# Performance work log

Hardware: AMD Instinct MI355X
Metric: run time of the kernel (lower is better)

The kernel has to match this reference:

```python
import jax, jax.numpy as jnp
import numpy as np

PT, SKIP, CNN_UNITS, RNN_UNITS = 16, 32, 512, 512


def setup_inputs() -> dict:
    key = jax.random.key(0)
    k_x, k_w, k_u = jax.random.split(key, 3)
    B, T, C, H = 128, 512, CNN_UNITS, RNN_UNITS
    # 0.05 scaling keeps the relu GRU recurrence numerically stable
    x = jax.random.normal(k_x, (B, T, C), dtype=jnp.float32)
    W = jax.random.normal(k_w, (C, 3 * H), dtype=jnp.float32) * 0.05
    U = jax.random.normal(k_u, (H, 3 * H), dtype=jnp.float32) * 0.05
    b = jnp.zeros((2, 3 * H), dtype=jnp.float32)  # [input_bias, recurrent_bias] (reset_after=True)
    return {"x": x, "W": W, "U": U, "b": b}


def reference(x, W, U, b):
    B, T, C = x.shape
    H = U.shape[0]
    pt, skip = PT, SKIP
    # pretrans: last pt*skip steps -> (B, pt, skip, C) -> (B, skip, pt, C) -> (B*skip, pt, C)
    s = x[:, -pt * skip:, :]
    s = s.reshape(B, pt, skip, C).transpose(0, 2, 1, 3).reshape(B * skip, pt, C)
    # precompute input projections for all timesteps: (pt, B*skip, 3H)
    xp = jnp.einsum('ntc,ch->tnh', s, W) + b[0]
    b_rec = b[1]

    def step(h, xt):
        rec = h @ U + b_rec                      # (N, 3H)
        xz, xr, xh = jnp.split(xt, 3, axis=-1)
        rz, rr, rh = jnp.split(rec, 3, axis=-1)
        z = jax.nn.sigmoid(xz + rz)
        r = jax.nn.sigmoid(xr + rr)
        hh = jax.nn.relu(xh + r * rh)            # activation='relu'
        h_new = z * h + (1.0 - z) * hh
        return h_new, None

    h0 = jnp.zeros((B * skip, H), dtype=x.dtype)
    h_final, _ = jax.lax.scan(step, h0, xp)
    # posttrans: (B*skip, H) -> (B, skip*H)
    return h_final.reshape(B, skip * H)
```

## Files before the change

### kernel.cpp

```cpp
#include <hip/hip_runtime.h>
#include <cstddef>


typedef unsigned short u16;
typedef __attribute__((ext_vector_type(8))) short short8;
typedef __attribute__((ext_vector_type(8))) u16 u16x8;
typedef __attribute__((ext_vector_type(4))) float floatx4;

#define MFMA16(a, b, c) __builtin_amdgcn_mfma_f32_16x16x32_bf16((a), (b), (c), 0, 0, 0)

__device__ __forceinline__ u16 f32_to_bf16(float f) {
  union { float f; unsigned int u; } c; c.f = f;
  unsigned int u = c.u + 0x7FFFu + ((c.u >> 16) & 1u);
  return (u16)(u >> 16);
}
__device__ __forceinline__ float bf16_to_f32(u16 v) {
  union { unsigned int u; float f; } c; c.u = ((unsigned int)v) << 16;
  return c.f;
}
__device__ __forceinline__ float sigmoidf_(float x) {
  return 1.0f / (1.0f + __expf(-x));
}
__device__ __forceinline__ void gload_lds16(const void* g, void* l) {
  __builtin_amdgcn_global_load_lds(
      (const __attribute__((address_space(1))) unsigned int*)g,
      (__attribute__((address_space(3))) unsigned int*)l, 16, 0, 0);
}

__global__ __launch_bounds__(256)
void pack_x(const float* __restrict__ x, u16* __restrict__ xb) {
  __shared__ u16 sm[64 * 512];
  const int t = blockIdx.x >> 6;
  const int nb = blockIdx.x & 63;
  const int tid = threadIdx.x;
#pragma unroll
  for (int it = 0; it < 16; ++it) {
    int idx = it * 256 + tid;
    int row = idx >> 6, ch = idx & 63;
    int xrow = (nb * 2 + (row >> 5)) * 512 + t * 32 + (row & 31);
    const float* src = x + (size_t)xrow * 512 + ch * 8;
    floatx4 va = *(const floatx4*)src;
    floatx4 vb = *(const floatx4*)(src + 4);
    u16x8 pk;
    pk[0] = f32_to_bf16(va[0]); pk[1] = f32_to_bf16(va[1]);
    pk[2] = f32_to_bf16(va[2]); pk[3] = f32_to_bf16(va[3]);
    pk[4] = f32_to_bf16(vb[0]); pk[5] = f32_to_bf16(vb[1]);
    pk[6] = f32_to_bf16(vb[2]); pk[7] = f32_to_bf16(vb[3]);
    *(u16x8*)&sm[row * 512 + (ch ^ (row & 7)) * 8] = pk;
  }
  __syncthreads();
  u16* dst = xb + (size_t)blockIdx.x * 32768;
#pragma unroll
  for (int it = 0; it < 16; ++it) {
    int idx = it * 256 + tid;
    int row = idx & 63, g = (idx >> 6) & 3, kt = idx >> 8;
    int ch = kt * 4 + g;
    u16x8 vv = *(const u16x8*)&sm[row * 512 + (ch ^ (row & 7)) * 8];
    *(u16x8*)(dst + (size_t)idx * 8) = vv;
  }
}

__global__ void pack_Bt(const float* __restrict__ W, const float* __restrict__ U,
                        u16* __restrict__ Bt) {
  size_t gid = (size_t)blockIdx.x * 256 + threadIdx.x;
  int col = (int)(gid & 63);
  int g   = (int)((gid >> 6) & 3);
  int kt  = (int)((gid >> 8) & 31);
  int cc  = (int)(gid >> 13);
  int c = cc * 64 + col;
  int k0 = kt * 32 + g * 8;
  u16x8 pk;
#pragma unroll
  for (int j = 0; j < 8; ++j) {
    int k = k0 + j;
    float v = (k < 512) ? W[(size_t)k * 1536 + c] : U[(size_t)(k - 512) * 1536 + c];
    pk[j] = f32_to_bf16(v);
  }
  *(u16x8*)(Bt + gid * 8) = pk;
}

__global__ __launch_bounds__(256)
void gru_step(const u16* __restrict__ xb, const u16* __restrict__ Bt,
              const float* __restrict__ bias,
              const u16* __restrict__ h_in, u16* __restrict__ h_out,
              float* __restrict__ out, int t, int first, int last) {
  __shared__ alignas(16) char sm[65536];
  const int tid = threadIdx.x;
  const int idx = blockIdx.x;
  const int nb = ((idx >> 6) << 3) | (idx & 7);
  const int hb = (idx >> 3) & 7;
  const int w = __builtin_amdgcn_readfirstlane(tid >> 6);
  const int lane = tid & 63;
  const int wy = w >> 1, wx = w & 1;
  const int q = lane >> 4, lc = lane & 15;

  const u16* xbB = xb + (size_t)(t * 64 + nb) * 32768;
  const u16* htB = h_in + (size_t)nb * 32768;
  const int cs0 = hb, cs1 = 8 + hb, cs2 = 16 + hb;

  floatx4 acZ[2][2] = {{{0.f,0.f,0.f,0.f},{0.f,0.f,0.f,0.f}},{{0.f,0.f,0.f,0.f},{0.f,0.f,0.f,0.f}}};
  floatx4 acR[2][2] = {{{0.f,0.f,0.f,0.f},{0.f,0.f,0.f,0.f}},{{0.f,0.f,0.f,0.f},{0.f,0.f,0.f,0.f}}};
  floatx4 acX[2][2] = {{{0.f,0.f,0.f,0.f},{0.f,0.f,0.f,0.f}},{{0.f,0.f,0.f,0.f},{0.f,0.f,0.f,0.f}}};
  floatx4 acH[2][2] = {{{0.f,0.f,0.f,0.f},{0.f,0.f,0.f,0.f}},{{0.f,0.f,0.f,0.f},{0.f,0.f,0.f,0.f}}};

  const int wo = w * 1024;

  auto stage = [&](int kt, int bsel) {
    char* lds = sm + bsel * 16384;
    const char* aS = (const char*)((kt < 16) ? (xbB + (size_t)kt * 2048)
                                             : (htB + (size_t)(kt - 16) * 2048));
    gload_lds16(aS + wo + lane * 16, lds + wo);
    gload_lds16((const char*)(Bt + (size_t)(cs0 * 32 + kt) * 2048) + wo + lane * 16,
                lds + 4096 + wo);
    gload_lds16((const char*)(Bt + (size_t)(cs1 * 32 + kt) * 2048) + wo + lane * 16,
                lds + 8192 + wo);
    gload_lds16((const char*)(Bt + (size_t)(cs2 * 32 + kt) * 2048) + wo + lane * 16,
                lds + 12288 + wo);
  };

  auto compute = [&](int bsel, floatx4 (&acT)[2][2]) {
    const char* lds = sm + bsel * 16384;
    short8 a0 = *(const short8*)(lds + (q * 64 + wy * 32 + lc) * 16);
    short8 a1 = *(const short8*)(lds + (q * 64 + wy * 32 + 16 + lc) * 16);
#pragma unroll
    for (int ci = 0; ci < 2; ++ci) {
      int co = (q * 64 + wx * 32 + ci * 16 + lc) * 16;
      short8 bz = *(const short8*)(lds + 4096 + co);
      short8 br = *(const short8*)(lds + 8192 + co);
      short8 bh = *(const short8*)(lds + 12288 + co);
      acZ[0][ci] = MFMA16(a0, bz, acZ[0][ci]);
      acZ[1][ci] = MFMA16(a1, bz, acZ[1][ci]);
      acR[0][ci] = MFMA16(a0, br, acR[0][ci]);
      acR[1][ci] = MFMA16(a1, br, acR[1][ci]);
      acT[0][ci] = MFMA16(a0, bh, acT[0][ci]);
      acT[1][ci] = MFMA16(a1, bh, acT[1][ci]);
    }
  };

  stage(0, 0);
  stage(1, 1);
  stage(2, 2);
  if (first) {
    for (int kt = 0; kt < 14; ++kt) {
      asm volatile("s_waitcnt vmcnt(8)" ::: "memory");
      __builtin_amdgcn_s_barrier();
      if (kt < 13) stage(kt + 3, (kt + 3) & 3);
      __builtin_amdgcn_s_setprio(1);
      compute(kt & 3, acX);
      __builtin_amdgcn_s_setprio(0);
    }
    asm volatile("s_waitcnt vmcnt(4)" ::: "memory");
    __builtin_amdgcn_s_barrier();
    __builtin_amdgcn_s_setprio(1);
    compute(2, acX);
    __builtin_amdgcn_s_setprio(0);
    asm volatile("s_waitcnt vmcnt(0)" ::: "memory");
    __builtin_amdgcn_s_barrier();
    __builtin_amdgcn_s_setprio(1);
    compute(3, acX);
    __builtin_amdgcn_s_setprio(0);
  } else {
    for (int kt = 0; kt < 16; ++kt) {
      asm volatile("s_waitcnt vmcnt(8)" ::: "memory");
      __builtin_amdgcn_s_barrier();
      stage(kt + 3, (kt + 3) & 3);
      __builtin_amdgcn_s_setprio(1);
      compute(kt & 3, acX);
      __builtin_amdgcn_s_setprio(0);
    }
    for (int kt = 16; kt < 30; ++kt) {
      asm volatile("s_waitcnt vmcnt(8)" ::: "memory");
      __builtin_amdgcn_s_barrier();
      if (kt < 29) stage(kt + 3, (kt + 3) & 3);
      __builtin_amdgcn_s_setprio(1);
      compute(kt & 3, acH);
      __builtin_amdgcn_s_setprio(0);
    }
    asm volatile("s_waitcnt vmcnt(4)" ::: "memory");
    __builtin_amdgcn_s_barrier();
    __builtin_amdgcn_s_setprio(1);
    compute(2, acH);
    __builtin_amdgcn_s_setprio(0);
    asm volatile("s_waitcnt vmcnt(0)" ::: "memory");
    __builtin_amdgcn_s_barrier();
    __builtin_amdgcn_s_setprio(1);
    compute(3, acH);
    __builtin_amdgcn_s_setprio(0);
  }

  __syncthreads();
  const float* b0 = bias;
  const float* b1 = bias + 1536;
  u16* Ct = (u16*)sm;
#pragma unroll
  for (int ci = 0; ci < 2; ++ci) {
    const int hcl = wx * 32 + ci * 16 + lc;
    const int hg = hb * 64 + hcl;
    const float bz = b0[hg] + b1[hg];
    const float br = b0[512 + hg] + b1[512 + hg];
    const float b0h = b0[1024 + hg];
    const float b1h = b1[1024 + hg];
    const int ktg = hg >> 5;
    const int gg = (hg >> 3) & 3;
    const size_t hbase = (((size_t)nb * 16 + ktg) * 4 + gg) * 64;
#pragma unroll
    for (int mi = 0; mi < 2; ++mi) {
#pragma unroll
      for (int reg = 0; reg < 4; ++reg) {
        const int nl = wy * 32 + mi * 16 + q * 4 + reg;
        const int n = nb * 64 + nl;
        float z = sigmoidf_(acZ[mi][ci][reg] + bz);
        float r = sigmoidf_(acR[mi][ci][reg] + br);
        float hh = acX[mi][ci][reg] + b0h + r * (acH[mi][ci][reg] + b1h);
        hh = fmaxf(hh, 0.0f);
        float hp = 0.0f;
        if (!first) hp = bf16_to_f32(h_in[(hbase + nl) * 8 + (hg & 7)]);
        float v = z * hp + (1.0f - z) * hh;
        if (last) out[(size_t)n * 512 + hg] = v;
        else      Ct[nl * 72 + hcl] = f32_to_bf16(v);
      }
    }
  }
  if (!last) {
    __syncthreads();
#pragma unroll
    for (int i = 0; i < 2; ++i) {
      int e = i * 256 + tid;
      int row = e & 63;
      int g = (e >> 6) & 3;
      int ktl = e >> 8;
      u16x8 vv = *(const u16x8*)(Ct + row * 72 + ktl * 32 + g * 8);
      *(u16x8*)(h_out + ((((size_t)nb * 16 + (hb * 2 + ktl)) * 4 + g) * 64 + row) * 8) = vv;
    }
  }
}

extern "C" void kernel_launch(void* const* d_in, const int* in_sizes, int n_in,
                              void* d_out, int out_size, void* d_ws, size_t ws_size,
                              hipStream_t stream) {
  const float* x = (const float*)d_in[0];
  const float* W = (const float*)d_in[1];
  const float* U = (const float*)d_in[2];
  const float* bias = (const float*)d_in[3];
  float* out = (float*)d_out;

  u16* xb = (u16*)d_ws;
  u16* Bt = xb + (size_t)16 * 64 * 32768;
  u16* h0 = Bt + (size_t)1536 * 1024;
  u16* h1 = h0 + (size_t)4096 * 512;

  pack_x<<<1024, 256, 0, stream>>>(x, xb);
  pack_Bt<<<768, 256, 0, stream>>>(W, U, Bt);

  for (int t = 0; t < 16; ++t) {
    const u16* hin = (t & 1) ? h1 : h0;
    u16* hout = (t & 1) ? h0 : h1;
    gru_step<<<512, 256, 0, stream>>>(
        xb, Bt, bias, hin, hout, out, t, (t == 0) ? 1 : 0, (t == 15) ? 1 : 0);
  }
}
```

Baseline: 503.6 us.

## Hoist input projection into one batched GEMM before recurrent steps

Moves the x·W input projection for all 16 timesteps out of the sequential per-step kernels into a single large 8192-block GEMM that writes fp32 results to workspace. Each gru_step then only does the h·U recurrent GEMM (K=512 instead of 1024) and reads the precomputed projections in its epilogue. This gives the input GEMM full-GPU parallelism instead of 512 blocks per step, and halves the serial critical path. The cost is an extra fp32 intermediate buffer (about 400MB written and read back) and the assumption that the workspace is large enough to hold it.

```diff
diff --git a/kernel.cpp b/kernel.cpp
--- a/kernel.cpp
+++ b/kernel.cpp
@@ -80,8 +80,94 @@
 }
 
 __global__ __launch_bounds__(256)
-void gru_step(const u16* __restrict__ xb, const u16* __restrict__ Bt,
-              const float* __restrict__ bias,
+void xw_gemm(const u16* __restrict__ xb, const u16* __restrict__ Bt,
+             float* __restrict__ xp) {
+  __shared__ alignas(16) char sm[65536];
+  const int tid = threadIdx.x;
+  const int xcd = blockIdx.x & 7;
+  const int g8  = blockIdx.x >> 3;
+  const int hb  = g8 & 7;
+  const int tn  = (g8 >> 3) * 8 + xcd;
+  const int w = __builtin_amdgcn_readfirstlane(tid >> 6);
+  const int lane = tid & 63;
+  const int wy = w >> 1, wx = w & 1;
+  const int q = lane >> 4, lc = lane & 15;
+
+  const u16* aB = xb + (size_t)tn * 32768;
+  const int cs0 = hb, cs1 = 8 + hb, cs2 = 16 + hb;
+
+  floatx4 acZ[2][2] = {{{0.f,0.f,0.f,0.f},{0.f,0.f,0.f,0.f}},{{0.f,0.f,0.f,0.f},{0.f,0.f,0.f,0.f}}};
+  floatx4 acR[2][2] = {{{0.f,0.f,0.f,0.f},{0.f,0.f,0.f,0.f}},{{0.f,0.f,0.f,0.f},{0.f,0.f,0.f,0.f}}};
+  floatx4 acX[2][2] = {{{0.f,0.f,0.f,0.f},{0.f,0.f,0.f,0.f}},{{0.f,0.f,0.f,0.f},{0.f,0.f,0.f,0.f}}};
+
+  const int wo = w * 1024;
+
+  auto stage = [&](int kt, int bsel) {
+    char* lds = sm + bsel * 16384;
+    gload_lds16((const char*)(aB + (size_t)kt * 2048) + wo + lane * 16, lds + wo);
+    gload_lds16((const char*)(Bt + (size_t)(cs0 * 32 + kt) * 2048) + wo + lane * 16,
+                lds + 4096 + wo);
+    gload_lds16((const char*)(Bt + (size_t)(cs1 * 32 + kt) * 2048) + wo + lane * 16,
+                lds + 8192 + wo);
+    gload_lds16((const char*)(Bt + (size_t)(cs2 * 32 + kt) * 2048) + wo + lane * 16,
+                lds + 12288 + wo);
+  };
+
+  auto compute = [&](int slot) {
+    const char* lds = sm + slot * 16384;
+    short8 a0 = *(const short8*)(lds + (q * 64 + wy * 32 + lc) * 16);
+    short8 a1 = *(const short8*)(lds + (q * 64 + wy * 32 + 16 + lc) * 16);
+#pragma unroll
+    for (int ci = 0; ci < 2; ++ci) {
+      int co = (q * 64 + wx * 32 + ci * 16 + lc) * 16;
+      short8 bz = *(const short8*)(lds + 4096 + co);
+      short8 br = *(const short8*)(lds + 8192 + co);
+      short8 bh = *(const short8*)(lds + 12288 + co);
+      acZ[0][ci] = MFMA16(a0, bz, acZ[0][ci]);
+      acZ[1][ci] = MFMA16(a1, bz, acZ[1][ci]);
+      acR[0][ci] = MFMA16(a0, br, acR[0][ci]);
+      acR[1][ci] = MFMA16(a1, br, acR[1][ci]);
+      acX[0][ci] = MFMA16(a0, bh, acX[0][ci]);
+      acX[1][ci] = MFMA16(a1, bh, acX[1][ci]);
+    }
+  };
+
+  stage(0, 0); stage(1, 1); stage(2, 2);
+  for (int kt = 0; kt < 14; ++kt) {
+    asm volatile("s_waitcnt vmcnt(8)" ::: "memory");
+    __builtin_amdgcn_s_barrier();
+    if (kt < 13) stage(kt + 3, (kt + 3) & 3);
+    __builtin_amdgcn_s_setprio(1);
+    compute(kt & 3);
+    __builtin_amdgcn_s_setprio(0);
+  }
+  asm volatile("s_waitcnt vmcnt(4)" ::: "memory");
+  __builtin_amdgcn_s_barrier();
+  __builtin_amdgcn_s_setprio(1);
+  compute(2);
+  __builtin_amdgcn_s_setprio(0);
+  asm volatile("s_waitcnt vmcnt(0)" ::: "memory");
+  __builtin_amdgcn_s_barrier();
+  __builtin_amdgcn_s_setprio(1);
+  compute(3);
+  __builtin_amdgcn_s_setprio(0);
+
+  const size_t bp = (size_t)tn * 8 + hb;
+  float* base = xp + (bp * 12) * 1024;
+#pragma unroll
+  for (int mi = 0; mi < 2; ++mi)
+#pragma unroll
+    for (int ci = 0; ci < 2; ++ci) {
+      int j = mi * 2 + ci;
+      *(floatx4*)(base + (size_t)(0 * 4 + j) * 1024 + tid * 4) = acZ[mi][ci];
+      *(floatx4*)(base + (size_t)(1 * 4 + j) * 1024 + tid * 4) = acR[mi][ci];
+      *(floatx4*)(base + (size_t)(2 * 4 + j) * 1024 + tid * 4) = acX[mi][ci];
+    }
+}
+
+__global__ __launch_bounds__(256)
+void gru_step(const u16* __restrict__ Bt, const float* __restrict__ bias,
+              const float* __restrict__ xp,
               const u16* __restrict__ h_in, u16* __restrict__ h_out,
               float* __restrict__ out, int t, int first, int last) {
   __shared__ alignas(16) char sm[65536];
@@ -94,32 +180,28 @@
   const int wy = w >> 1, wx = w & 1;
   const int q = lane >> 4, lc = lane & 15;
 
-  const u16* xbB = xb + (size_t)(t * 64 + nb) * 32768;
   const u16* htB = h_in + (size_t)nb * 32768;
   const int cs0 = hb, cs1 = 8 + hb, cs2 = 16 + hb;
 
   floatx4 acZ[2][2] = {{{0.f,0.f,0.f,0.f},{0.f,0.f,0.f,0.f}},{{0.f,0.f,0.f,0.f},{0.f,0.f,0.f,0.f}}};
   floatx4 acR[2][2] = {{{0.f,0.f,0.f,0.f},{0.f,0.f,0.f,0.f}},{{0.f,0.f,0.f,0.f},{0.f,0.f,0.f,0.f}}};
-  floatx4 acX[2][2] = {{{0.f,0.f,0.f,0.f},{0.f,0.f,0.f,0.f}},{{0.f,0.f,0.f,0.f},{0.f,0.f,0.f,0.f}}};
   floatx4 acH[2][2] = {{{0.f,0.f,0.f,0.f},{0.f,0.f,0.f,0.f}},{{0.f,0.f,0.f,0.f},{0.f,0.f,0.f,0.f}}};
 
   const int wo = w * 1024;
 
   auto stage = [&](int kt, int bsel) {
     char* lds = sm + bsel * 16384;
-    const char* aS = (const char*)((kt < 16) ? (xbB + (size_t)kt * 2048)
-                                             : (htB + (size_t)(kt - 16) * 2048));
-    gload_lds16(aS + wo + lane * 16, lds + wo);
-    gload_lds16((const char*)(Bt + (size_t)(cs0 * 32 + kt) * 2048) + wo + lane * 16,
+    gload_lds16((const char*)(htB + (size_t)kt * 2048) + wo + lane * 16, lds + wo);
+    gload_lds16((const char*)(Bt + (size_t)(cs0 * 32 + 16 + kt) * 2048) + wo + lane * 16,
                 lds + 4096 + wo);
-    gload_lds16((const char*)(Bt + (size_t)(cs1 * 32 + kt) * 2048) + wo + lane * 16,
+    gload_lds16((const char*)(Bt + (size_t)(cs1 * 32 + 16 + kt) * 2048) + wo + lane * 16,
                 lds + 8192 + wo);
-    gload_lds16((const char*)(Bt + (size_t)(cs2 * 32 + kt) * 2048) + wo + lane * 16,
+    gload_lds16((const char*)(Bt + (size_t)(cs2 * 32 + 16 + kt) * 2048) + wo + lane * 16,
                 lds + 12288 + wo);
   };
 
-  auto compute = [&](int bsel, floatx4 (&acT)[2][2]) {
-    const char* lds = sm + bsel * 16384;
+  auto compute = [&](int slot) {
+    const char* lds = sm + slot * 16384;
     short8 a0 = *(const short8*)(lds + (q * 64 + wy * 32 + lc) * 16);
     short8 a1 = *(const short8*)(lds + (q * 64 + wy * 32 + 16 + lc) * 16);
 #pragma unroll
@@ -132,63 +214,46 @@
       acZ[1][ci] = MFMA16(a1, bz, acZ[1][ci]);
       acR[0][ci] = MFMA16(a0, br, acR[0][ci]);
       acR[1][ci] = MFMA16(a1, br, acR[1][ci]);
-      acT[0][ci] = MFMA16(a0, bh, acT[0][ci]);
-      acT[1][ci] = MFMA16(a1, bh, acT[1][ci]);
+      acH[0][ci] = MFMA16(a0, bh, acH[0][ci]);
+      acH[1][ci] = MFMA16(a1, bh, acH[1][ci]);
     }
   };
 
-  stage(0, 0);
-  stage(1, 1);
-  stage(2, 2);
-  if (first) {
+  if (!first) {
+    stage(0, 0); stage(1, 1); stage(2, 2);
     for (int kt = 0; kt < 14; ++kt) {
       asm volatile("s_waitcnt vmcnt(8)" ::: "memory");
       __builtin_amdgcn_s_barrier();
       if (kt < 13) stage(kt + 3, (kt + 3) & 3);
       __builtin_amdgcn_s_setprio(1);
-      compute(kt & 3, acX);
+      compute(kt & 3);
       __builtin_amdgcn_s_setprio(0);
     }
     asm volatile("s_waitcnt vmcnt(4)" ::: "memory");
     __builtin_amdgcn_s_barrier();
     __builtin_amdgcn_s_setprio(1);
-    compute(2, acX);
+    compute(2);
     __builtin_amdgcn_s_setprio(0);
     asm volatile("s_waitcnt vmcnt(0)" ::: "memory");
     __builtin_amdgcn_s_barrier();
     __builtin_amdgcn_s_setprio(1);
-    compute(3, acX);
+    compute(3);
     __builtin_amdgcn_s_setprio(0);
-  } else {
-    for (int kt = 0; kt < 16; ++kt) {
-      asm volatile("s_waitcnt vmcnt(8)" ::: "memory");
-      __builtin_amdgcn_s_barrier();
-      stage(kt + 3, (kt + 3) & 3);
-      __builtin_amdgcn_s_setprio(1);
-      compute(kt & 3, acX);
-      __builtin_amdgcn_s_setprio(0);
-    }
-    for (int kt = 16; kt < 30; ++kt) {
-      asm volatile("s_waitcnt vmcnt(8)" ::: "memory");
-      __builtin_amdgcn_s_barrier();
-      if (kt < 29) stage(kt + 3, (kt + 3) & 3);
-      __builtin_amdgcn_s_setprio(1);
-      compute(kt & 3, acH);
-      __builtin_amdgcn_s_setprio(0);
-    }
-    asm volatile("s_waitcnt vmcnt(4)" ::: "memory");
-    __builtin_amdgcn_s_barrier();
-    __builtin_amdgcn_s_setprio(1);
-    compute(2, acH);
-    __builtin_amdgcn_s_setprio(0);
-    asm volatile("s_waitcnt vmcnt(0)" ::: "memory");
-    __builtin_amdgcn_s_barrier();
-    __builtin_amdgcn_s_setprio(1);
-    compute(3, acH);
-    __builtin_amdgcn_s_setprio(0);
   }
 
   __syncthreads();
+  const size_t bp = ((size_t)(t * 64 + nb)) * 8 + hb;
+  const float* xbase = xp + (bp * 12) * 1024;
+  floatx4 xpZ[2][2], xpR[2][2], xpX[2][2];
+#pragma unroll
+  for (int mi = 0; mi < 2; ++mi)
+#pragma unroll
+    for (int ci = 0; ci < 2; ++ci) {
+      int j = mi * 2 + ci;
+      xpZ[mi][ci] = *(const floatx4*)(xbase + (size_t)(0 * 4 + j) * 1024 + tid * 4);
+      xpR[mi][ci] = *(const floatx4*)(xbase + (size_t)(1 * 4 + j) * 1024 + tid * 4);
+      xpX[mi][ci] = *(const floatx4*)(xbase + (size_t)(2 * 4 + j) * 1024 + tid * 4);
+    }
   const float* b0 = bias;
   const float* b1 = bias + 1536;
   u16* Ct = (u16*)sm;
@@ -209,9 +274,9 @@
       for (int reg = 0; reg < 4; ++reg) {
         const int nl = wy * 32 + mi * 16 + q * 4 + reg;
         const int n = nb * 64 + nl;
-        float z = sigmoidf_(acZ[mi][ci][reg] + bz);
-        float r = sigmoidf_(acR[mi][ci][reg] + br);
-        float hh = acX[mi][ci][reg] + b0h + r * (acH[mi][ci][reg] + b1h);
+        float z = sigmoidf_(xpZ[mi][ci][reg] + acZ[mi][ci][reg] + bz);
+        float r = sigmoidf_(xpR[mi][ci][reg] + acR[mi][ci][reg] + br);
+        float hh = xpX[mi][ci][reg] + b0h + r * (acH[mi][ci][reg] + b1h);
         hh = fmaxf(hh, 0.0f);
         float hp = 0.0f;
         if (!first) hp = bf16_to_f32(h_in[(hbase + nl) * 8 + (hg & 7)]);
@@ -248,14 +313,16 @@
   u16* Bt = xb + (size_t)16 * 64 * 32768;
   u16* h0 = Bt + (size_t)1536 * 1024;
   u16* h1 = h0 + (size_t)4096 * 512;
+  float* xp = (float*)(h1 + (size_t)4096 * 512);
 
   pack_x<<<1024, 256, 0, stream>>>(x, xb);
   pack_Bt<<<768, 256, 0, stream>>>(W, U, Bt);
+  xw_gemm<<<8192, 256, 0, stream>>>(xb, Bt, xp);
 
   for (int t = 0; t < 16; ++t) {
     const u16* hin = (t & 1) ? h1 : h0;
     u16* hout = (t & 1) ? h0 : h1;
     gru_step<<<512, 256, 0, stream>>>(
-        xb, Bt, bias, hin, hout, out, t, (t == 0) ? 1 : 0, (t == 15) ? 1 : 0);
-  }
-}
+        Bt, bias, xp, hin, hout, out, t, (t == 0) ? 1 : 0, (t == 15) ? 1 : 0);
+  }
+}
```

Measured after the change: 657.9 us. 30.6% more time.

## Fuse all GRU timesteps into one persistent kernel with per-batch-group counters

Applied to the files above, without the earlier changes.

Replaces the 16 per-timestep launches with one kernel that loops over timesteps. Blocks that share a batch group of rows synchronise through an atomic counter, which is polled only just before the recurrent-state tiles are loaded. Each step's input-projection part (the first 16 K-tiles) can therefore start before the previous step's hidden state is ready, and launch gaps disappear. The scheme relies on all 512 blocks being co-resident, otherwise the spin-wait can deadlock, and the output staging buffer moves to a separate LDS region.

```diff
diff --git a/kernel.cpp b/kernel.cpp
--- a/kernel.cpp
+++ b/kernel.cpp
@@ -80,10 +80,10 @@
 }
 
 __global__ __launch_bounds__(256)
-void gru_step(const u16* __restrict__ xb, const u16* __restrict__ Bt,
-              const float* __restrict__ bias,
-              const u16* __restrict__ h_in, u16* __restrict__ h_out,
-              float* __restrict__ out, int t, int first, int last) {
+void gru_all(const u16* __restrict__ xb, const u16* __restrict__ Bt,
+             const float* __restrict__ bias,
+             u16* __restrict__ h0, u16* __restrict__ h1,
+             float* __restrict__ out, unsigned int* __restrict__ cnt) {
   __shared__ alignas(16) char sm[65536];
   const int tid = threadIdx.x;
   const int idx = blockIdx.x;
@@ -93,144 +93,180 @@
   const int lane = tid & 63;
   const int wy = w >> 1, wx = w & 1;
   const int q = lane >> 4, lc = lane & 15;
-
-  const u16* xbB = xb + (size_t)(t * 64 + nb) * 32768;
-  const u16* htB = h_in + (size_t)nb * 32768;
   const int cs0 = hb, cs1 = 8 + hb, cs2 = 16 + hb;
-
-  floatx4 acZ[2][2] = {{{0.f,0.f,0.f,0.f},{0.f,0.f,0.f,0.f}},{{0.f,0.f,0.f,0.f},{0.f,0.f,0.f,0.f}}};
-  floatx4 acR[2][2] = {{{0.f,0.f,0.f,0.f},{0.f,0.f,0.f,0.f}},{{0.f,0.f,0.f,0.f},{0.f,0.f,0.f,0.f}}};
-  floatx4 acX[2][2] = {{{0.f,0.f,0.f,0.f},{0.f,0.f,0.f,0.f}},{{0.f,0.f,0.f,0.f},{0.f,0.f,0.f,0.f}}};
-  floatx4 acH[2][2] = {{{0.f,0.f,0.f,0.f},{0.f,0.f,0.f,0.f}},{{0.f,0.f,0.f,0.f},{0.f,0.f,0.f,0.f}}};
-
   const int wo = w * 1024;
-
-  auto stage = [&](int kt, int bsel) {
-    char* lds = sm + bsel * 16384;
-    const char* aS = (const char*)((kt < 16) ? (xbB + (size_t)kt * 2048)
-                                             : (htB + (size_t)(kt - 16) * 2048));
-    gload_lds16(aS + wo + lane * 16, lds + wo);
-    gload_lds16((const char*)(Bt + (size_t)(cs0 * 32 + kt) * 2048) + wo + lane * 16,
-                lds + 4096 + wo);
-    gload_lds16((const char*)(Bt + (size_t)(cs1 * 32 + kt) * 2048) + wo + lane * 16,
-                lds + 8192 + wo);
-    gload_lds16((const char*)(Bt + (size_t)(cs2 * 32 + kt) * 2048) + wo + lane * 16,
-                lds + 12288 + wo);
-  };
-
-  auto compute = [&](int bsel, floatx4 (&acT)[2][2]) {
-    const char* lds = sm + bsel * 16384;
-    short8 a0 = *(const short8*)(lds + (q * 64 + wy * 32 + lc) * 16);
-    short8 a1 = *(const short8*)(lds + (q * 64 + wy * 32 + 16 + lc) * 16);
-#pragma unroll
-    for (int ci = 0; ci < 2; ++ci) {
-      int co = (q * 64 + wx * 32 + ci * 16 + lc) * 16;
-      short8 bz = *(const short8*)(lds + 4096 + co);
-      short8 br = *(const short8*)(lds + 8192 + co);
-      short8 bh = *(const short8*)(lds + 12288 + co);
-      acZ[0][ci] = MFMA16(a0, bz, acZ[0][ci]);
-      acZ[1][ci] = MFMA16(a1, bz, acZ[1][ci]);
-      acR[0][ci] = MFMA16(a0, br, acR[0][ci]);
-      acR[1][ci] = MFMA16(a1, br, acR[1][ci]);
-      acT[0][ci] = MFMA16(a0, bh, acT[0][ci]);
-      acT[1][ci] = MFMA16(a1, bh, acT[1][ci]);
-    }
-  };
-
-  stage(0, 0);
-  stage(1, 1);
-  stage(2, 2);
-  if (first) {
-    for (int kt = 0; kt < 14; ++kt) {
-      asm volatile("s_waitcnt vmcnt(8)" ::: "memory");
-      __builtin_amdgcn_s_barrier();
-      if (kt < 13) stage(kt + 3, (kt + 3) & 3);
-      __builtin_amdgcn_s_setprio(1);
-      compute(kt & 3, acX);
-      __builtin_amdgcn_s_setprio(0);
-    }
-    asm volatile("s_waitcnt vmcnt(4)" ::: "memory");
-    __builtin_amdgcn_s_barrier();
-    __builtin_amdgcn_s_setprio(1);
-    compute(2, acX);
-    __builtin_amdgcn_s_setprio(0);
-    asm volatile("s_waitcnt vmcnt(0)" ::: "memory");
-    __builtin_amdgcn_s_barrier();
-    __builtin_amdgcn_s_setprio(1);
-    compute(3, acX);
-    __builtin_amdgcn_s_setprio(0);
-  } else {
-    for (int kt = 0; kt < 16; ++kt) {
-      asm volatile("s_waitcnt vmcnt(8)" ::: "memory");
-      __builtin_amdgcn_s_barrier();
-      stage(kt + 3, (kt + 3) & 3);
-      __builtin_amdgcn_s_setprio(1);
-      compute(kt & 3, acX);
-      __builtin_amdgcn_s_setprio(0);
-    }
-    for (int kt = 16; kt < 30; ++kt) {
-      asm volatile("s_waitcnt vmcnt(8)" ::: "memory");
-      __builtin_amdgcn_s_barrier();
-      if (kt < 29) stage(kt + 3, (kt + 3) & 3);
-      __builtin_amdgcn_s_setprio(1);
-      compute(kt & 3, acH);
-      __builtin_amdgcn_s_setprio(0);
-    }
-    asm volatile("s_waitcnt vmcnt(4)" ::: "memory");
-    __builtin_amdgcn_s_barrier();
-    __builtin_amdgcn_s_setprio(1);
-    compute(2, acH);
-    __builtin_amdgcn_s_setprio(0);
-    asm volatile("s_waitcnt vmcnt(0)" ::: "memory");
-    __builtin_amdgcn_s_barrier();
-    __builtin_amdgcn_s_setprio(1);
-    compute(3, acH);
-    __builtin_amdgcn_s_setprio(0);
-  }
-
-  __syncthreads();
   const float* b0 = bias;
   const float* b1 = bias + 1536;
-  u16* Ct = (u16*)sm;
-#pragma unroll
-  for (int ci = 0; ci < 2; ++ci) {
-    const int hcl = wx * 32 + ci * 16 + lc;
-    const int hg = hb * 64 + hcl;
-    const float bz = b0[hg] + b1[hg];
-    const float br = b0[512 + hg] + b1[512 + hg];
-    const float b0h = b0[1024 + hg];
-    const float b1h = b1[1024 + hg];
-    const int ktg = hg >> 5;
-    const int gg = (hg >> 3) & 3;
-    const size_t hbase = (((size_t)nb * 16 + ktg) * 4 + gg) * 64;
-#pragma unroll
-    for (int mi = 0; mi < 2; ++mi) {
-#pragma unroll
-      for (int reg = 0; reg < 4; ++reg) {
-        const int nl = wy * 32 + mi * 16 + q * 4 + reg;
-        const int n = nb * 64 + nl;
-        float z = sigmoidf_(acZ[mi][ci][reg] + bz);
-        float r = sigmoidf_(acR[mi][ci][reg] + br);
-        float hh = acX[mi][ci][reg] + b0h + r * (acH[mi][ci][reg] + b1h);
-        hh = fmaxf(hh, 0.0f);
-        float hp = 0.0f;
-        if (!first) hp = bf16_to_f32(h_in[(hbase + nl) * 8 + (hg & 7)]);
-        float v = z * hp + (1.0f - z) * hh;
-        if (last) out[(size_t)n * 512 + hg] = v;
-        else      Ct[nl * 72 + hcl] = f32_to_bf16(v);
-      }
+  unsigned int* myc = cnt + nb;
+
+  for (int t = 0; t < 16; ++t) {
+    const int first = (t == 0) ? 1 : 0;
+    const int last  = (t == 15) ? 1 : 0;
+    const u16* hinF = (t & 1) ? h1 : h0;
+    u16* houtF      = (t & 1) ? h0 : h1;
+    const u16* xbB = xb + (size_t)(t * 64 + nb) * 32768;
+    const u16* htB = hinF + (size_t)nb * 32768;
+
+    floatx4 acZ[2][2] = {{{0.f,0.f,0.f,0.f},{0.f,0.f,0.f,0.f}},{{0.f,0.f,0.f,0.f},{0.f,0.f,0.f,0.f}}};
+    floatx4 acR[2][2] = {{{0.f,0.f,0.f,0.f},{0.f,0.f,0.f,0.f}},{{0.f,0.f,0.f,0.f},{0.f,0.f,0.f,0.f}}};
+    floatx4 acX[2][2] = {{{0.f,0.f,0.f,0.f},{0.f,0.f,0.f,0.f}},{{0.f,0.f,0.f,0.f},{0.f,0.f,0.f,0.f}}};
+    floatx4 acH[2][2] = {{{0.f,0.f,0.f,0.f},{0.f,0.f,0.f,0.f}},{{0.f,0.f,0.f,0.f},{0.f,0.f,0.f,0.f}}};
+
+    auto stage = [&](int kt) {
+      char* lds = sm + (kt & 3) * 16384;
+      const char* aS = (const char*)((kt < 16) ? (xbB + (size_t)kt * 2048)
+                                               : (htB + (size_t)(kt - 16) * 2048));
+      gload_lds16(aS + wo + lane * 16, lds + wo);
+      gload_lds16((const char*)(Bt + (size_t)(cs0 * 32 + kt) * 2048) + wo + lane * 16,
+                  lds + 4096 + wo);
+      gload_lds16((const char*)(Bt + (size_t)(cs1 * 32 + kt) * 2048) + wo + lane * 16,
+                  lds + 8192 + wo);
+      gload_lds16((const char*)(Bt + (size_t)(cs2 * 32 + kt) * 2048) + wo + lane * 16,
+                  lds + 12288 + wo);
+    };
+    auto compute = [&](int slot, floatx4 (&acT)[2][2]) {
+      const char* lds = sm + slot * 16384;
+      short8 a0 = *(const short8*)(lds + (q * 64 + wy * 32 + lc) * 16);
+      short8 a1 = *(const short8*)(lds + (q * 64 + wy * 32 + 16 + lc) * 16);
+#pragma unroll
+      for (int ci = 0; ci < 2; ++ci) {
+        int co = (q * 64 + wx * 32 + ci * 16 + lc) * 16;
+        short8 bz = *(const short8*)(lds + 4096 + co);
+        short8 br = *(const short8*)(lds + 8192 + co);
+        short8 bh = *(const short8*)(lds + 12288 + co);
+        acZ[0][ci] = MFMA16(a0, bz, acZ[0][ci]);
+        acZ[1][ci] = MFMA16(a1, bz, acZ[1][ci]);
+        acR[0][ci] = MFMA16(a0, br, acR[0][ci]);
+        acR[1][ci] = MFMA16(a1, br, acR[1][ci]);
+        acT[0][ci] = MFMA16(a0, bh, acT[0][ci]);
+        acT[1][ci] = MFMA16(a1, bh, acT[1][ci]);
+      }
+    };
+
+    stage(0); stage(1); stage(2);
+    if (first) {
+      for (int kt = 0; kt < 14; ++kt) {
+        asm volatile("s_waitcnt vmcnt(8)" ::: "memory");
+        __builtin_amdgcn_s_barrier();
+        if (kt < 13) stage(kt + 3);
+        __builtin_amdgcn_s_setprio(1);
+        compute(kt & 3, acX);
+        __builtin_amdgcn_s_setprio(0);
+      }
+      asm volatile("s_waitcnt vmcnt(4)" ::: "memory");
+      __builtin_amdgcn_s_barrier();
+      __builtin_amdgcn_s_setprio(1);
+      compute(2, acX);
+      __builtin_amdgcn_s_setprio(0);
+      asm volatile("s_waitcnt vmcnt(0)" ::: "memory");
+      __builtin_amdgcn_s_barrier();
+      __builtin_amdgcn_s_setprio(1);
+      compute(3, acX);
+      __builtin_amdgcn_s_setprio(0);
+    } else {
+      for (int kt = 0; kt < 13; ++kt) {
+        asm volatile("s_waitcnt vmcnt(8)" ::: "memory");
+        __builtin_amdgcn_s_barrier();
+        stage(kt + 3);
+        __builtin_amdgcn_s_setprio(1);
+        compute(kt & 3, acX);
+        __builtin_amdgcn_s_setprio(0);
+      }
+      asm volatile("s_waitcnt vmcnt(8)" ::: "memory");
+      __builtin_amdgcn_s_barrier();
+      {
+        const unsigned int tgt = 8u * (unsigned int)t;
+        while (__hip_atomic_load(myc, __ATOMIC_ACQUIRE,
+                                 __HIP_MEMORY_SCOPE_AGENT) < tgt)
+          __builtin_amdgcn_s_sleep(2);
+      }
+      stage(16);
+      __builtin_amdgcn_s_setprio(1);
+      compute(1, acX);
+      __builtin_amdgcn_s_setprio(0);
+      asm volatile("s_waitcnt vmcnt(8)" ::: "memory");
+      __builtin_amdgcn_s_barrier();
+      stage(17);
+      __builtin_amdgcn_s_setprio(1);
+      compute(2, acX);
+      __builtin_amdgcn_s_setprio(0);
+      asm volatile("s_waitcnt vmcnt(8)" ::: "memory");
+      __builtin_amdgcn_s_barrier();
+      stage(18);
+      __builtin_amdgcn_s_setprio(1);
+      compute(3, acX);
+      __builtin_amdgcn_s_setprio(0);
+      for (int kt = 16; kt < 29; ++kt) {
+        asm volatile("s_waitcnt vmcnt(8)" ::: "memory");
+        __builtin_amdgcn_s_barrier();
+        stage(kt + 3);
+        __builtin_amdgcn_s_setprio(1);
+        compute(kt & 3, acH);
+        __builtin_amdgcn_s_setprio(0);
+      }
+      asm volatile("s_waitcnt vmcnt(8)" ::: "memory");
+      __builtin_amdgcn_s_barrier();
+      __builtin_amdgcn_s_setprio(1);
+      compute(1, acH);
+      __builtin_amdgcn_s_setprio(0);
+      asm volatile("s_waitcnt vmcnt(4)" ::: "memory");
+      __builtin_amdgcn_s_barrier();
+      __builtin_amdgcn_s_setprio(1);
+      compute(2, acH);
+      __builtin_amdgcn_s_setprio(0);
+      asm volatile("s_waitcnt vmcnt(0)" ::: "memory");
+      __builtin_amdgcn_s_barrier();
+      __builtin_amdgcn_s_setprio(1);
+      compute(3, acH);
+      __builtin_amdgcn_s_setprio(0);
     }
-  }
-  if (!last) {
+
     __syncthreads();
-#pragma unroll
-    for (int i = 0; i < 2; ++i) {
-      int e = i * 256 + tid;
-      int row = e & 63;
-      int g = (e >> 6) & 3;
-      int ktl = e >> 8;
-      u16x8 vv = *(const u16x8*)(Ct + row * 72 + ktl * 32 + g * 8);
-      *(u16x8*)(h_out + ((((size_t)nb * 16 + (hb * 2 + ktl)) * 4 + g) * 64 + row) * 8) = vv;
+    u16* Ct = (u16*)(sm + 49152);
+#pragma unroll
+    for (int ci = 0; ci < 2; ++ci) {
+      const int hcl = wx * 32 + ci * 16 + lc;
+      const int hg = hb * 64 + hcl;
+      const float bz = b0[hg] + b1[hg];
+      const float br = b0[512 + hg] + b1[512 + hg];
+      const float b0h = b0[1024 + hg];
+      const float b1h = b1[1024 + hg];
+      const int ktg = hg >> 5;
+      const int gg = (hg >> 3) & 3;
+      const size_t hbase = (((size_t)nb * 16 + ktg) * 4 + gg) * 64;
+#pragma unroll
+      for (int mi = 0; mi < 2; ++mi) {
+#pragma unroll
+        for (int reg = 0; reg < 4; ++reg) {
+          const int nl = wy * 32 + mi * 16 + q * 4 + reg;
+          const int n = nb * 64 + nl;
+          float z = sigmoidf_(acZ[mi][ci][reg] + bz);
+          float r = sigmoidf_(acR[mi][ci][reg] + br);
+          float hh = acX[mi][ci][reg] + b0h + r * (acH[mi][ci][reg] + b1h);
+          hh = fmaxf(hh, 0.0f);
+          float hp = 0.0f;
+          if (!first) hp = bf16_to_f32(hinF[(hbase + nl) * 8 + (hg & 7)]);
+          float v = z * hp + (1.0f - z) * hh;
+          if (last) out[(size_t)n * 512 + hg] = v;
+          else      Ct[nl * 72 + hcl] = f32_to_bf16(v);
+        }
+      }
+    }
+    if (!last) {
+      __syncthreads();
+#pragma unroll
+      for (int i = 0; i < 2; ++i) {
+        int e = i * 256 + tid;
+        int row = e & 63;
+        int g = (e >> 6) & 3;
+        int ktl = e >> 8;
+        u16x8 vv = *(const u16x8*)(Ct + row * 72 + ktl * 32 + g * 8);
+        *(u16x8*)(houtF + ((((size_t)nb * 16 + (hb * 2 + ktl)) * 4 + g) * 64 + row) * 8) = vv;
+      }
+      __syncthreads();
+      if (tid == 0)
+        __hip_atomic_fetch_add(myc, 1u, __ATOMIC_RELEASE,
+                               __HIP_MEMORY_SCOPE_AGENT);
     }
   }
 }
@@ -248,14 +284,10 @@
   u16* Bt = xb + (size_t)16 * 64 * 32768;
   u16* h0 = Bt + (size_t)1536 * 1024;
   u16* h1 = h0 + (size_t)4096 * 512;
-
+  unsigned int* cnt = (unsigned int*)(h1 + (size_t)4096 * 512);
+
+  hipMemsetAsync(cnt, 0, 64 * sizeof(unsigned int), stream);
   pack_x<<<1024, 256, 0, stream>>>(x, xb);
   pack_Bt<<<768, 256, 0, stream>>>(W, U, Bt);
-
-  for (int t = 0; t < 16; ++t) {
-    const u16* hin = (t & 1) ? h1 : h0;
-    u16* hout = (t & 1) ? h0 : h1;
-    gru_step<<<512, 256, 0, stream>>>(
-        xb, Bt, bias, hin, hout, out, t, (t == 0) ? 1 : 0, (t == 15) ? 1 : 0);
-  }
-}
+  gru_all<<<512, 256, 0, stream>>>(xb, Bt, bias, h0, h1, out, cnt);
+}
```

Result: slower. 943.5 us (+87.3%).

## Double GRU step block tile to 128 rows with triple-buffered LDS staging

Applied to the files above, without the earlier changes.

Each block now computes 128 batch rows instead of 64 against the same 64-column slice of the three gates. Weight tiles are therefore reused across twice as many rows, and the launch drops from 512 to 256 blocks. The LDS pipeline moves from four 16KB stages to three 20KB stages with adjusted waitcnt depth, and each wave holds twice as many MFMA accumulators. The risks are lower occupancy (about one block per CU), higher register pressure, and a shallower prefetch pipeline to hide global-to-LDS latency.

```diff
diff --git a/kernel.cpp b/kernel.cpp
--- a/kernel.cpp
+++ b/kernel.cpp
@@ -84,107 +84,124 @@
               const float* __restrict__ bias,
               const u16* __restrict__ h_in, u16* __restrict__ h_out,
               float* __restrict__ out, int t, int first, int last) {
-  __shared__ alignas(16) char sm[65536];
+  __shared__ alignas(16) char sm[61440];
   const int tid = threadIdx.x;
   const int idx = blockIdx.x;
-  const int nb = ((idx >> 6) << 3) | (idx & 7);
-  const int hb = (idx >> 3) & 7;
+  const int nbb = ((idx >> 6) << 3) | (idx & 7);
+  const int hb  = (idx >> 3) & 7;
   const int w = __builtin_amdgcn_readfirstlane(tid >> 6);
   const int lane = tid & 63;
   const int wy = w >> 1, wx = w & 1;
   const int q = lane >> 4, lc = lane & 15;
 
-  const u16* xbB = xb + (size_t)(t * 64 + nb) * 32768;
-  const u16* htB = h_in + (size_t)nb * 32768;
-  const int cs0 = hb, cs1 = 8 + hb, cs2 = 16 + hb;
-
-  floatx4 acZ[2][2] = {{{0.f,0.f,0.f,0.f},{0.f,0.f,0.f,0.f}},{{0.f,0.f,0.f,0.f},{0.f,0.f,0.f,0.f}}};
-  floatx4 acR[2][2] = {{{0.f,0.f,0.f,0.f},{0.f,0.f,0.f,0.f}},{{0.f,0.f,0.f,0.f},{0.f,0.f,0.f,0.f}}};
-  floatx4 acX[2][2] = {{{0.f,0.f,0.f,0.f},{0.f,0.f,0.f,0.f}},{{0.f,0.f,0.f,0.f},{0.f,0.f,0.f,0.f}}};
-  floatx4 acH[2][2] = {{{0.f,0.f,0.f,0.f},{0.f,0.f,0.f,0.f}},{{0.f,0.f,0.f,0.f},{0.f,0.f,0.f,0.f}}};
-
-  const int wo = w * 1024;
-
-  auto stage = [&](int kt, int bsel) {
-    char* lds = sm + bsel * 16384;
-    const char* aS = (const char*)((kt < 16) ? (xbB + (size_t)kt * 2048)
-                                             : (htB + (size_t)(kt - 16) * 2048));
-    gload_lds16(aS + wo + lane * 16, lds + wo);
-    gload_lds16((const char*)(Bt + (size_t)(cs0 * 32 + kt) * 2048) + wo + lane * 16,
-                lds + 4096 + wo);
-    gload_lds16((const char*)(Bt + (size_t)(cs1 * 32 + kt) * 2048) + wo + lane * 16,
-                lds + 8192 + wo);
-    gload_lds16((const char*)(Bt + (size_t)(cs2 * 32 + kt) * 2048) + wo + lane * 16,
-                lds + 12288 + wo);
+  const u16* xbB = xb + (size_t)(t * 64 + nbb * 2) * 32768;
+  const u16* htB = h_in + (size_t)(nbb * 2) * 32768;
+
+  floatx4 acZ[4][2], acR[4][2], acX[4][2], acH[4][2];
+#pragma unroll
+  for (int f = 0; f < 4; ++f)
+#pragma unroll
+    for (int ci = 0; ci < 2; ++ci) {
+      acZ[f][ci] = (floatx4){0.f, 0.f, 0.f, 0.f};
+      acR[f][ci] = (floatx4){0.f, 0.f, 0.f, 0.f};
+      acX[f][ci] = (floatx4){0.f, 0.f, 0.f, 0.f};
+      acH[f][ci] = (floatx4){0.f, 0.f, 0.f, 0.f};
+    }
+
+  auto stage = [&](int kt, int slot) {
+    char* L = sm + slot * 20480;
+#pragma unroll
+    for (int i = 0; i < 5; ++i) {
+      int p = i * 4 + w;
+      const u16* src;
+      if (p < 8) {
+        int ah = p >> 2, g = p & 3;
+        src = (kt < 16)
+                ? xbB + (size_t)ah * 32768 + (size_t)kt * 2048 + (size_t)g * 512
+                : htB + (size_t)ah * 32768 + (size_t)(kt - 16) * 2048 + (size_t)g * 512;
+      } else {
+        int gate = (p - 8) >> 2, g = (p - 8) & 3;
+        int cs = gate * 8 + hb;
+        src = Bt + (size_t)(cs * 32 + kt) * 2048 + (size_t)g * 512;
+      }
+      gload_lds16((const char*)src + lane * 16, L + p * 1024);
+    }
   };
 
-  auto compute = [&](int bsel, floatx4 (&acT)[2][2]) {
-    const char* lds = sm + bsel * 16384;
-    short8 a0 = *(const short8*)(lds + (q * 64 + wy * 32 + lc) * 16);
-    short8 a1 = *(const short8*)(lds + (q * 64 + wy * 32 + 16 + lc) * 16);
+  auto compute = [&](int slot, floatx4 (&acT)[4][2]) {
+    const char* L = sm + slot * 20480;
+    const char* Ab = L + wy * 4096 + (q * 64 + lc) * 16;
+    short8 a0 = *(const short8*)(Ab);
+    short8 a1 = *(const short8*)(Ab + 256);
+    short8 a2 = *(const short8*)(Ab + 512);
+    short8 a3 = *(const short8*)(Ab + 768);
 #pragma unroll
     for (int ci = 0; ci < 2; ++ci) {
-      int co = (q * 64 + wx * 32 + ci * 16 + lc) * 16;
-      short8 bz = *(const short8*)(lds + 4096 + co);
-      short8 br = *(const short8*)(lds + 8192 + co);
-      short8 bh = *(const short8*)(lds + 12288 + co);
+      const char* Bb = L + 8192 + (q * 64 + wx * 32 + ci * 16 + lc) * 16;
+      short8 bz = *(const short8*)(Bb);
+      short8 br = *(const short8*)(Bb + 4096);
+      short8 bh = *(const short8*)(Bb + 8192);
       acZ[0][ci] = MFMA16(a0, bz, acZ[0][ci]);
       acZ[1][ci] = MFMA16(a1, bz, acZ[1][ci]);
+      acZ[2][ci] = MFMA16(a2, bz, acZ[2][ci]);
+      acZ[3][ci] = MFMA16(a3, bz, acZ[3][ci]);
       acR[0][ci] = MFMA16(a0, br, acR[0][ci]);
       acR[1][ci] = MFMA16(a1, br, acR[1][ci]);
+      acR[2][ci] = MFMA16(a2, br, acR[2][ci]);
+      acR[3][ci] = MFMA16(a3, br, acR[3][ci]);
       acT[0][ci] = MFMA16(a0, bh, acT[0][ci]);
       acT[1][ci] = MFMA16(a1, bh, acT[1][ci]);
+      acT[2][ci] = MFMA16(a2, bh, acT[2][ci]);
+      acT[3][ci] = MFMA16(a3, bh, acT[3][ci]);
     }
   };
 
-  stage(0, 0);
-  stage(1, 1);
-  stage(2, 2);
+  stage(0, 0); stage(1, 1);
   if (first) {
     for (int kt = 0; kt < 14; ++kt) {
-      asm volatile("s_waitcnt vmcnt(8)" ::: "memory");
+      asm volatile("s_waitcnt vmcnt(5)" ::: "memory");
       __builtin_amdgcn_s_barrier();
-      if (kt < 13) stage(kt + 3, (kt + 3) & 3);
+      if (kt < 14) stage(kt + 2, (kt + 2) % 3);
       __builtin_amdgcn_s_setprio(1);
-      compute(kt & 3, acX);
+      compute(kt % 3, acX);
       __builtin_amdgcn_s_setprio(0);
     }
-    asm volatile("s_waitcnt vmcnt(4)" ::: "memory");
-    __builtin_amdgcn_s_barrier();
-    __builtin_amdgcn_s_setprio(1);
-    compute(2, acX);
+    asm volatile("s_waitcnt vmcnt(5)" ::: "memory");
+    __builtin_amdgcn_s_barrier();
+    __builtin_amdgcn_s_setprio(1);
+    compute(14 % 3, acX);
     __builtin_amdgcn_s_setprio(0);
     asm volatile("s_waitcnt vmcnt(0)" ::: "memory");
     __builtin_amdgcn_s_barrier();
     __builtin_amdgcn_s_setprio(1);
-    compute(3, acX);
+    compute(15 % 3, acX);
     __builtin_amdgcn_s_setprio(0);
   } else {
     for (int kt = 0; kt < 16; ++kt) {
-      asm volatile("s_waitcnt vmcnt(8)" ::: "memory");
+      asm volatile("s_waitcnt vmcnt(5)" ::: "memory");
       __builtin_amdgcn_s_barrier();
-      stage(kt + 3, (kt + 3) & 3);
+      stage(kt + 2, (kt + 2) % 3);
       __builtin_amdgcn_s_setprio(1);
-      compute(kt & 3, acX);
+      compute(kt % 3, acX);
       __builtin_amdgcn_s_setprio(0);
     }
     for (int kt = 16; kt < 30; ++kt) {
-      asm volatile("s_waitcnt vmcnt(8)" ::: "memory");
+      asm volatile("s_waitcnt vmcnt(5)" ::: "memory");
       __builtin_amdgcn_s_barrier();
-      if (kt < 29) stage(kt + 3, (kt + 3) & 3);
+      stage(kt + 2, (kt + 2) % 3);
       __builtin_amdgcn_s_setprio(1);
-      compute(kt & 3, acH);
+      compute(kt % 3, acH);
       __builtin_amdgcn_s_setprio(0);
     }
-    asm volatile("s_waitcnt vmcnt(4)" ::: "memory");
-    __builtin_amdgcn_s_barrier();
-    __builtin_amdgcn_s_setprio(1);
-    compute(2, acH);
+    asm volatile("s_waitcnt vmcnt(5)" ::: "memory");
+    __builtin_amdgcn_s_barrier();
+    __builtin_amdgcn_s_setprio(1);
+    compute(30 % 3, acH);
     __builtin_amdgcn_s_setprio(0);
     asm volatile("s_waitcnt vmcnt(0)" ::: "memory");
     __builtin_amdgcn_s_barrier();
     __builtin_amdgcn_s_setprio(1);
-    compute(3, acH);
+    compute(31 % 3, acH);
     __builtin_amdgcn_s_setprio(0);
   }
 
@@ -202,19 +219,21 @@
     const float b1h = b1[1024 + hg];
     const int ktg = hg >> 5;
     const int gg = (hg >> 3) & 3;
-    const size_t hbase = (((size_t)nb * 16 + ktg) * 4 + gg) * 64;
-#pragma unroll
-    for (int mi = 0; mi < 2; ++mi) {
+    const int nb2 = nbb * 2 + wy;
+    const size_t hbase = (((size_t)nb2 * 16 + ktg) * 4 + gg) * 64;
+#pragma unroll
+    for (int f = 0; f < 4; ++f) {
 #pragma unroll
       for (int reg = 0; reg < 4; ++reg) {
-        const int nl = wy * 32 + mi * 16 + q * 4 + reg;
-        const int n = nb * 64 + nl;
-        float z = sigmoidf_(acZ[mi][ci][reg] + bz);
-        float r = sigmoidf_(acR[mi][ci][reg] + br);
-        float hh = acX[mi][ci][reg] + b0h + r * (acH[mi][ci][reg] + b1h);
+        const int rowl = f * 16 + q * 4 + reg;
+        const int nl = wy * 64 + rowl;
+        const int n = nbb * 128 + nl;
+        float z = sigmoidf_(acZ[f][ci][reg] + bz);
+        float r = sigmoidf_(acR[f][ci][reg] + br);
+        float hh = acX[f][ci][reg] + b0h + r * (acH[f][ci][reg] + b1h);
         hh = fmaxf(hh, 0.0f);
         float hp = 0.0f;
-        if (!first) hp = bf16_to_f32(h_in[(hbase + nl) * 8 + (hg & 7)]);
+        if (!first) hp = bf16_to_f32(h_in[(hbase + rowl) * 8 + (hg & 7)]);
         float v = z * hp + (1.0f - z) * hh;
         if (last) out[(size_t)n * 512 + hg] = v;
         else      Ct[nl * 72 + hcl] = f32_to_bf16(v);
@@ -224,13 +243,14 @@
   if (!last) {
     __syncthreads();
 #pragma unroll
-    for (int i = 0; i < 2; ++i) {
+    for (int i = 0; i < 4; ++i) {
       int e = i * 256 + tid;
-      int row = e & 63;
-      int g = (e >> 6) & 3;
-      int ktl = e >> 8;
-      u16x8 vv = *(const u16x8*)(Ct + row * 72 + ktl * 32 + g * 8);
-      *(u16x8*)(h_out + ((((size_t)nb * 16 + (hb * 2 + ktl)) * 4 + g) * 64 + row) * 8) = vv;
+      int row = e & 127, gc = e >> 7;
+      u16x8 vv = *(const u16x8*)(Ct + row * 72 + gc * 8);
+      int nb2 = nbb * 2 + (row >> 6);
+      int ktg = hb * 2 + (gc >> 2);
+      int g = gc & 3;
+      *(u16x8*)(h_out + ((((size_t)nb2 * 16 + ktg) * 4 + g) * 64 + (row & 63)) * 8) = vv;
     }
   }
 }
@@ -255,7 +275,7 @@
   for (int t = 0; t < 16; ++t) {
     const u16* hin = (t & 1) ? h1 : h0;
     u16* hout = (t & 1) ? h0 : h1;
-    gru_step<<<512, 256, 0, stream>>>(
+    gru_step<<<256, 256, 0, stream>>>(
         xb, Bt, bias, hin, hout, out, t, (t == 0) ? 1 : 0, (t == 15) ? 1 : 0);
   }
 }
```

New measurement: 602.3 us. 1.2x slower.
